# Performance work log

Hardware: AMD Instinct MI355X
Metric: run time of the kernel (lower is better)

The kernel has to match this reference:

```python
import jax, jax.numpy as jnp
import numpy as np
import math

GR = 24
NUM_TDFS = 6
DK = 32
F = 512
BN_UNITS = 192  # max(512*6 // 16, 16)
GROUPS = 4      # mk_norm_2d(24, 'gn') -> largest divisor of 24 in range(ceil(sqrt(24)),2,-1) = 4
EPS = 1e-5


def group_norm(x, w, b):
    # x: [B, C, H, W]; GroupNorm(GROUPS, C)
    B, C, H, W = x.shape
    xg = x.reshape(B, GROUPS, C // GROUPS, H, W)
    mu = xg.mean(axis=(2, 3, 4), keepdims=True)
    var = xg.var(axis=(2, 3, 4), keepdims=True)
    xn = ((xg - mu) * jax.lax.rsqrt(var + EPS)).reshape(B, C, H, W)
    return xn * w[None, :, None, None] + b[None, :, None, None]


def conv_block(x, w, b, gw, gb):
    # Conv2d 3x3 same padding, then GroupNorm, then ReLU
    y = jax.lax.conv_general_dilated(
        x, w, window_strides=(1, 1), padding=((1, 1), (1, 1)),
        dimension_numbers=('NCHW', 'OIHW', 'NCHW')) + b[None, :, None, None]
    return jax.nn.relu(group_norm(y, gw, gb))


def setup_inputs() -> dict:
    key = jax.random.key(0)
    ks = jax.random.split(key, 16)
    B, C_in, T = 4, 24, 128

    def glorot(k, shape, fan_in):
        return jax.random.normal(k, shape, jnp.float32) * (1.0 / math.sqrt(fan_in))

    inp = {
        'x': jax.random.normal(ks[0], (B, C_in, T, F), jnp.float32),
        'c': jax.random.normal(ks[1], (B, 32), jnp.float32),
        # TFC dense conv stack: in-channels 24, 48, 72 -> gr=24 each
        'conv_w0': glorot(ks[2], (GR, 24, 3, 3), 24 * 9), 'conv_b0': jnp.zeros((GR,), jnp.float32),
        'gn_w0': jnp.ones((GR,), jnp.float32), 'gn_b0': jnp.zeros((GR,), jnp.float32),
        'conv_w1': glorot(ks[3], (GR, 48, 3, 3), 48 * 9), 'conv_b1': jnp.zeros((GR,), jnp.float32),
        'gn_w1': jnp.ones((GR,), jnp.float32), 'gn_b1': jnp.zeros((GR,), jnp.float32),
        'conv_w2': glorot(ks[4], (GR, 72, 3, 3), 72 * 9), 'conv_b2': jnp.zeros((GR,), jnp.float32),
        'gn_w2': jnp.ones((GR,), jnp.float32), 'gn_b2': jnp.zeros((GR,), jnp.float32),
        # TDF bottleneck MLP (bias=False): f -> bn_units -> f*num_tdfs
        'tdf_w1': glorot(ks[5], (BN_UNITS, F), F),
        'tdf_gn1_w': jnp.ones((GR,), jnp.float32), 'tdf_gn1_b': jnp.zeros((GR,), jnp.float32),
        'tdf_w2': glorot(ks[6], (F * NUM_TDFS, BN_UNITS), BN_UNITS),
        'tdf_gn2_w': jnp.ones((GR,), jnp.float32), 'tdf_gn2_b': jnp.zeros((GR,), jnp.float32),
        # routing path
        'wq': glorot(ks[7], (DK, 32), 32), 'bq': jnp.zeros((DK,), jnp.float32),
        'keys': jax.random.normal(ks[8], (DK, NUM_TDFS), jnp.float32),
    }
    return inp


def reference(x, c,
              conv_w0, conv_b0, gn_w0, gn_b0,
              conv_w1, conv_b1, gn_w1, gn_b1,
              conv_w2, conv_b2, gn_w2, gn_b2,
              tdf_w1, tdf_gn1_w, tdf_gn1_b,
              tdf_w2, tdf_gn2_w, tdf_gn2_b,
              wq, bq, keys):
    # ---- TFC: densely connected conv blocks ----
    feat = conv_block(x, conv_w0, conv_b0, gn_w0, gn_b0)          # [B,gr,T,F]
    cat = jnp.concatenate([feat, x], axis=1)                      # [B,48,T,F]
    feat = conv_block(cat, conv_w1, conv_b1, gn_w1, gn_b1)
    cat = jnp.concatenate([feat, cat], axis=1)                    # [B,72,T,F]
    x_ = conv_block(cat, conv_w2, conv_b2, gn_w2, gn_b2)          # [B,gr,T,F]

    # ---- TDF bank: f -> bn_units -> f*num_tdfs (bias-free MLP with GN+ReLU) ----
    h = jnp.einsum('bctf,uf->bctu', x_, tdf_w1)                   # [B,gr,T,bn_units]
    h = jax.nn.relu(group_norm(h, tdf_gn1_w, tdf_gn1_b))
    h = jnp.einsum('bctu,ou->bcto', h, tdf_w2)                    # [B,gr,T,f*num_tdfs]
    h = jax.nn.relu(group_norm(h, tdf_gn2_w, tdf_gn2_b))
    B, gr, T, _ = h.shape
    value = h.reshape(B, gr, T, F, NUM_TDFS)                      # [B,gr,T,f,n]

    # ---- LaSAFT attention over TDF 'experts' ----
    q = c @ wq.T + bq                                             # [B,dk]
    att = jax.nn.softmax((q @ keys) / math.sqrt(DK), axis=-1)     # [B,n]
    mixed = jnp.einsum('bctfn,bn->bctf', value, att)              # [B,gr,T,f]
    return x_ + mixed
```

## Files before the change

kernel.cpp:

```cpp
#include <hip/hip_runtime.h>
#include <hip/hip_bf16.h>

typedef unsigned short u16;
typedef unsigned int u32;

#define Tn 128
#define Fn 512
#define HWc (Tn*Fn)
#define EPS 1e-5f

using bf16x8 = __attribute__((ext_vector_type(8))) short;
using f32x4  = __attribute__((ext_vector_type(4))) float;

__device__ __forceinline__ float b2f(u16 x){ return __uint_as_float(((u32)x)<<16); }
__device__ __forceinline__ u16 f2b(float f){
  __hip_bfloat16 h = __float2bfloat16(f);
  return *reinterpret_cast<u16*>(&h);
}

__device__ __forceinline__ void gload16(const u16* g, u16* l){
  __builtin_amdgcn_global_load_lds((const __attribute__((address_space(1))) void*)g,
                                   (__attribute__((address_space(3))) void*)l, 16, 0, 0);
}

__global__ void zero_stats2(float* a, float* b){
  int i = threadIdx.x;
  if (i < 128) a[i] = 0.f;
  else if (i < 160) b[i-128] = 0.f;
}

__global__ __launch_bounds__(256) void border_zero(u16* __restrict__ p, int CS){
  int b = blockIdx.y;
  u16* base = p + (long)b*130*514*CS;
  int rowN = 514*CS;
  for (int i = blockIdx.x*256 + threadIdx.x; i < rowN; i += gridDim.x*256){
    base[i] = 0;
    base[(long)129*rowN + i] = 0;
  }
  int colN = 128*CS;
  for (int i = blockIdx.x*256 + threadIdx.x; i < colN; i += gridDim.x*256){
    int row = 1 + i/CS, ch = i - (i/CS)*CS;
    base[((long)row*514 + 0)*CS + ch] = 0;
    base[((long)row*514 + 513)*CS + ch] = 0;
  }
}

__global__ __launch_bounds__(256) void cvt_f2b(const float* __restrict__ src, u16* __restrict__ dst){
  int i = (blockIdx.x*256 + threadIdx.x)*4;
  float4 v = *(const float4*)(src + i);
  ushort4 o;
  o.x=f2b(v.x); o.y=f2b(v.y); o.z=f2b(v.z); o.w=f2b(v.w);
  *(ushort4*)(dst + i) = o;
}

__global__ __launch_bounds__(256)
void prep_wr(const float* __restrict__ w, u16* __restrict__ wr,
             int CIN, int cs, int cof, int KP){
  int i = blockIdx.x*256 + threadIdx.x;
  int tot = 96*KP;
  if (i >= tot) return;
  int e  = i & 7;
  int r  = (i >> 3) & 15;
  int h  = (i >> 7) & 1;
  int q  = (i >> 8) & 3;
  int rest = i >> 10;
  int NK = KP >> 5;
  int ks = rest % NK, dt = rest / NK;
  int o = h*16 + r;
  int k = ks*32 + q*8 + e;
  float v = 0.f;
  int g = cof + k, df = g/cs, ch = g - df*cs;
  if (o < 24 && df < 3 && ch >= cof && ch < cof+CIN)
    v = w[((o*CIN + (ch-cof))*3 + dt)*3 + df];
  wr[i] = f2b(v);
}

__global__ __launch_bounds__(256)
void copy_x2(const float* __restrict__ x, u16* __restrict__ b72p, u16* __restrict__ xc24){
  __shared__ u16 sh[24][520];
  int t = blockIdx.x & 127, b = blockIdx.x >> 7;
  const float* src = x + ((long)(b*24)*128 + t)*512;
  for (int c=0; c<24; c++){
    float2 v = *(const float2*)(src + (long)c*65536 + threadIdx.x*2);
    sh[c][threadIdx.x*2]   = f2b(v.x);
    sh[c][threadIdx.x*2+1] = f2b(v.y);
  }
  __syncthreads();
  long r72 = ((long)(b*130 + t+1))*514*72;
  long r24 = ((long)(b*130 + t+1))*514*24;
  for (int i = threadIdx.x; i < 1536; i += 256){
    int f = i/3, c0 = (i%3)*8;
    union {int4 q; u16 u[8];} o;
    #pragma unroll
    for (int j=0;j<8;j++) o.u[j] = sh[c0+j][f];
    *(int4*)(b72p + r72 + (long)(f+1)*72 + 48 + c0) = o.q;
    *(int4*)(xc24 + r24 + (long)(f+1)*24 + c0) = o.q;
  }
}

template<int KP, int CS>
__global__ __launch_bounds__(256)
void conv_mfma(const u16* __restrict__ X, int coff, const u16* __restrict__ WR,
               const float* __restrict__ bias, u16* __restrict__ Y,
               float* __restrict__ raw){
  constexpr int NK = KP/32;
  __shared__ u16 WS[3*32*KP];
  __shared__ float ssum[4][32], ssq[4][32];
  __shared__ float g24s[24], g24q[24];
  __shared__ __align__(16) u16 Ysh[128*24];
  int bid = (blockIdx.x & 7)*64 + (blockIdx.x >> 3);
  int b = bid >> 7, t = bid & 127;
  int tid = threadIdx.x, wid = tid >> 6, l = tid & 63;
  int r = l & 15, q = l >> 4;

  for (int i = tid*8; i < 3*32*KP; i += 2048)
    *(int4*)(WS + i) = *(const int4*)(WR + i);

  float bv0 = bias[r];
  float bv1 = (r < 8) ? bias[16+r] : 0.f;
  float s0=0,q0=0,s1=0,q1=0;
  __syncthreads();

  #pragma unroll
  for (int fi=0; fi<4; fi++){
    int f0w = fi*128 + wid*32;
    f32x4 acc[2][2] = {};
    #pragma unroll
    for (int dt=0; dt<3; dt++){
      const u16* Ab = X + ((long)((b*130 + t+dt)*514 + f0w + r))*CS + coff + q*8;
      bf16x8 a[2][NK];
      #pragma unroll
      for (int ks=0; ks<NK; ks++){
        a[0][ks] = *(const bf16x8*)(Ab + ks*32);
        a[1][ks] = *(const bf16x8*)(Ab + (long)16*CS + ks*32);
      }
      #pragma unroll
      for (int ks=0; ks<NK; ks++){
        const u16* Bb = WS + ((dt*NK + ks)*4 + q)*256 + r*8;
        bf16x8 b0 = *(const bf16x8*)(Bb);
        bf16x8 b1 = *(const bf16x8*)(Bb + 128);
        acc[0][0] = __builtin_amdgcn_mfma_f32_16x16x32_bf16(a[0][ks],b0,acc[0][0],0,0,0);
        acc[0][1] = __builtin_amdgcn_mfma_f32_16x16x32_bf16(a[0][ks],b1,acc[0][1],0,0,0);
        acc[1][0] = __builtin_amdgcn_mfma_f32_16x16x32_bf16(a[1][ks],b0,acc[1][0],0,0,0);
        acc[1][1] = __builtin_amdgcn_mfma_f32_16x16x32_bf16(a[1][ks],b1,acc[1][1],0,0,0);
      }
    }
    #pragma unroll
    for (int m=0;m<2;m++){
      #pragma unroll
      for (int j=0;j<4;j++){
        acc[m][0][j] += bv0; acc[m][1][j] += bv1;
        s0 += acc[m][0][j]; q0 += acc[m][0][j]*acc[m][0][j];
        s1 += acc[m][1][j]; q1 += acc[m][1][j]*acc[m][1][j];
      }
    }
    __syncthreads();
    #pragma unroll
    for (int m=0;m<2;m++){
      int fr = wid*32 + m*16 + q*4;
      #pragma unroll
      for (int j=0;j<4;j++){
        Ysh[(fr+j)*24 + r] = f2b(acc[m][0][j]);
        if (r < 8) Ysh[(fr+j)*24 + 16 + r] = f2b(acc[m][1][j]);
      }
    }
    __syncthreads();
    long Yb = ((long)((b*128 + t)*512) + fi*128)*24;
    const int4* sp = (const int4*)Ysh;
    for (int i = tid; i < 384; i += 256)
      *(int4*)(Y + Yb + (long)i*8) = sp[i];
  }

  #pragma unroll
  for (int off=16; off<=32; off<<=1){
    s0 += __shfl_xor(s0, off, 64); q0 += __shfl_xor(q0, off, 64);
    s1 += __shfl_xor(s1, off, 64); q1 += __shfl_xor(q1, off, 64);
  }
  if (q == 0){
    ssum[wid][r] = s0;     ssq[wid][r] = q0;
    ssum[wid][16+r] = s1;  ssq[wid][16+r] = q1;
  }
  __syncthreads();
  if (tid < 24){
    g24s[tid] = ssum[0][tid]+ssum[1][tid]+ssum[2][tid]+ssum[3][tid];
    g24q[tid] = ssq[0][tid]+ssq[1][tid]+ssq[2][tid]+ssq[3][tid];
  }
  __syncthreads();
  if (tid < 4){
    float as=0, aq=0;
    #pragma unroll
    for (int j=0;j<6;j++){ as += g24s[tid*6+j]; aq += g24q[tid*6+j]; }
    atomicAdd(&raw[b*4+tid], as);
    atomicAdd(&raw[16+b*4+tid], aq);
  }
}

__global__ __launch_bounds__(256)
void norm_relu_nhwc(const u16* __restrict__ Y, u16* __restrict__ dst, int coff,
                    const float* __restrict__ raw, const float* __restrict__ gw,
                    const float* __restrict__ gb, float invN){
  __shared__ float sA[24], sB[24];
  int bb = blockIdx.x / 768;
  if (threadIdx.x < 24){
    int g = bb*4 + threadIdx.x/6;
    float m = raw[g]*invN;
    float var = raw[16+g]*invN - m*m;
    float is = rsqrtf(var + EPS);
    float sc = is*gw[threadIdx.x];
    sA[threadIdx.x] = sc;
    sB[threadIdx.x] = gb[threadIdx.x] - m*sc;
  }
  __syncthreads();
  long e = ((long)blockIdx.x*256 + threadIdx.x)*8;
  int c0 = (int)(e % 24);
  long fi = e / 24;
  int f = (int)(fi & 511);
  int bt = (int)(fi >> 9); int t = bt & 127, b = bt >> 7;
  union {int4 q; u16 u[8];} pk; pk.q = *(const int4*)(Y + e);
  union {int4 q; u16 u[8];} o;
  #pragma unroll
  for (int j=0;j<8;j++){
    float v = b2f(pk.u[j])*sA[c0+j] + sB[c0+j];
    o.u[j] = f2b(v>0.f?v:0.f);
  }
  *(int4*)(dst + ((long)(b*130 + t+1)*514 + (f+1))*72 + coff + c0) = o.q;
}

__global__ __launch_bounds__(256)
void norm_relu_chw(const u16* __restrict__ Y, u16* __restrict__ xr,
                   const float* __restrict__ raw, const float* __restrict__ gw,
                   const float* __restrict__ gb, float invN){
  __shared__ u16 sh[24][520];
  __shared__ float sA[24], sB[24];
  int t = blockIdx.x & 127, b = blockIdx.x >> 7;
  if (threadIdx.x < 24){
    int g = b*4 + threadIdx.x/6;
    float m = raw[g]*invN;
    float var = raw[16+g]*invN - m*m;
    float is = rsqrtf(var + EPS);
    float sc = is*gw[threadIdx.x];
    sA[threadIdx.x] = sc;
    sB[threadIdx.x] = gb[threadIdx.x] - m*sc;
  }
  __syncthreads();
  const u16* src = Y + ((long)(b*128+t))*12288;
  for (int i = threadIdx.x; i < 1536; i += 256){
    int e = i*8; int c0 = e % 24; int f = e / 24;
    union {int4 q; u16 u[8];} pk; pk.q = *(const int4*)(src + e);
    #pragma unroll
    for (int j=0;j<8;j++){
      float v = b2f(pk.u[j])*sA[c0+j] + sB[c0+j];
      sh[c0+j][f] = f2b(v>0.f?v:0.f);
    }
  }
  __syncthreads();
  for (int i = threadIdx.x; i < 1536; i += 256){
    int c = i >> 6, fq = (i & 63)*8;
    union {int4 q; u16 u[8];} o;
    #pragma unroll
    for (int j=0;j<8;j++) o.u[j] = sh[c][fq+j];
    *(int4*)(xr + ((long)((b*24+c)*128 + t))*512 + fq) = o.q;
  }
}

__global__ __launch_bounds__(256)
void norm_chw(u16* __restrict__ h, const float* __restrict__ raw,
              const float* __restrict__ gw, const float* __restrict__ gb, float invN){
  __shared__ float s_sc, s_off;
  int bc = blockIdx.x / 12;
  if (threadIdx.x == 0){
    int b = bc/24, c = bc%24;
    int g = b*4 + c/6;
    float m = raw[g]*invN;
    float var = raw[16+g]*invN - m*m;
    float is = rsqrtf(var + EPS);
    float sc = is*gw[c];
    s_sc = sc;
    s_off = gb[c] - m*sc;
  }
  __syncthreads();
  float sc = s_sc, off = s_off;
  long e = ((long)blockIdx.x*256 + threadIdx.x)*8;
  union {int4 q; u16 u[8];} pk; pk.q = *(const int4*)(h + e);
  #pragma unroll
  for (int j=0;j<8;j++){ float v = b2f(pk.u[j])*sc + off; pk.u[j] = f2b(v>0.f?v:0.f); }
  *(int4*)(h + e) = pk.q;
}

template<int NF, bool STORE>
__global__ __launch_bounds__(256)
void gemm_lds(const u16* __restrict__ A, const u16* __restrict__ Bt, u16* __restrict__ C,
              int N, int K, int NBX, float* __restrict__ raw){
  constexpr int BN = NF*32;
  constexpr int BNP = BN + 4;
  constexpr int ABUF = 128*32;
  constexpr int BBUF = BN*32;
  __shared__ __align__(16) u16 SH[3*(ABUF+BBUF)];
  u16* Asb = SH;
  u16* Bsb = SH + 3*ABUF;
  int tid = threadIdx.x, wid = tid >> 6, l = tid & 63;
  int r = l & 15, q = l >> 4;
  int wr = wid >> 1, wc = wid & 1;
  int chunk = gridDim.x >> 3;
  int lin = (blockIdx.x & 7)*chunk + (blockIdx.x >> 3);
  int bx = lin % NBX, by = lin / NBX;
  long m0 = (long)by*128;
  int n0 = bx*BN;

  int arow[2], ach[2], aslot[2];
  #pragma unroll
  for (int j=0;j<2;j++){
    int idx = (wid*2+j)*64 + l;
    aslot[j] = idx*8;
    arow[j]  = ((idx>>6)<<4) | (idx & 15);
    ach[j]   = ((idx>>4) & 3)*8;
  }
  int brow[NF/2], bch[NF/2], bslot[NF/2];
  #pragma unroll
  for (int j=0;j<NF/2;j++){
    int idx = (wid*(NF/2)+j)*64 + l;
    bslot[j] = idx*8;
    brow[j]  = ((idx>>6)<<4) | (idx & 15);
    bch[j]   = ((idx>>4) & 3)*8;
  }

  f32x4 acc[4][NF];
  #pragma unroll
  for (int mf=0;mf<4;mf++)
    #pragma unroll
    for (int nf=0;nf<NF;nf++) acc[mf][nf] = (f32x4){0.f,0.f,0.f,0.f};

  int nt = K >> 5;
  #pragma unroll
  for (int j=0;j<2;j++)    gload16(A  + (m0+arow[j])*K + ach[j], Asb + aslot[j]);
  #pragma unroll
  for (int j=0;j<NF/2;j++) gload16(Bt + (long)(n0+brow[j])*K + bch[j], Bsb + bslot[j]);
  #pragma unroll
  for (int j=0;j<2;j++)    gload16(A  + (m0+arow[j])*K + 32 + ach[j], Asb + ABUF + aslot[j]);
  #pragma unroll
  for (int j=0;j<NF/2;j++) gload16(Bt + (long)(n0+brow[j])*K + 32 + bch[j], Bsb + BBUF + bslot[j]);

  int c0 = 0;
  for (int kt=0; kt<nt; kt++){
    if constexpr (NF==4) asm volatile("s_waitcnt vmcnt(4)" ::: "memory");
    else                 asm volatile("s_waitcnt vmcnt(3)" ::: "memory");
    __builtin_amdgcn_s_barrier();
    __builtin_amdgcn_sched_barrier(0);
    if (kt+2 < nt){
      int c2 = c0+2; if (c2>=3) c2-=3;
      int ko = (kt+2)*32;
      #pragma unroll
      for (int j=0;j<2;j++)    gload16(A  + (m0+arow[j])*K + ko + ach[j], Asb + c2*ABUF + aslot[j]);
      #pragma unroll
      for (int j=0;j<NF/2;j++) gload16(Bt + (long)(n0+brow[j])*K + ko + bch[j], Bsb + c2*BBUF + bslot[j]);
    }
    const u16* Ac = Asb + c0*ABUF;
    const u16* Bc = Bsb + c0*BBUF;
    bf16x8 af[4], bfv[NF];
    #pragma unroll
    for (int mf=0;mf<4;mf++) af[mf]  = *(const bf16x8*)(Ac + (((wr*4+mf)*4 + q)*16 + r)*8);
    #pragma unroll
    for (int nf=0;nf<NF;nf++) bfv[nf] = *(const bf16x8*)(Bc + (((wc*NF+nf)*4 + q)*16 + r)*8);
    #pragma unroll
    for (int mf=0;mf<4;mf++)
      #pragma unroll
      for (int nf=0;nf<NF;nf++)
        acc[mf][nf] = __builtin_amdgcn_mfma_f32_16x16x32_bf16(af[mf], bfv[nf], acc[mf][nf], 0,0,0);
    c0 = (c0+1==3) ? 0 : c0+1;
  }

  float s=0.f, ss=0.f;
  #pragma unroll
  for (int mf=0;mf<4;mf++)
    #pragma unroll
    for (int nf=0;nf<NF;nf++)
      #pragma unroll
      for (int j=0;j<4;j++){ float v = acc[mf][nf][j]; s += v; ss += v*v; }
  #pragma unroll
  for (int off=32; off>0; off>>=1){ s += __shfl_down(s,off,64); ss += __shfl_down(ss,off,64); }
  __shared__ float rs[4], rss[4];
  if (l==0){ rs[wid]=s; rss[wid]=ss; }
  __syncthreads();
  if (tid==0){
    int bc = (int)(m0 >> 7);
    int g = (bc/24)*4 + (bc%24)/6;
    atomicAdd(&raw[g],    rs[0]+rs[1]+rs[2]+rs[3]);
    atomicAdd(&raw[16+g], rss[0]+rss[1]+rss[2]+rss[3]);
  }

  if constexpr (STORE){
    #pragma unroll
    for (int mf=0;mf<4;mf++){
      int row = wr*64 + mf*16 + q*4;
      #pragma unroll
      for (int nf=0;nf<NF;nf++){
        int col = wc*(NF*16) + nf*16 + r;
        #pragma unroll
        for (int j=0;j<4;j++)
          SH[(row+j)*BNP + col] = f2b(acc[mf][nf][j]);
      }
    }
    __syncthreads();
    constexpr int RPT = BN/16;
    #pragma unroll
    for (int k=0;k<RPT;k++){
      int j = tid + k*256;
      int row = j / (BN/8), col8 = (j % (BN/8))*8;
      *(int4*)(C + (m0+row)*N + n0 + col8) = *(const int4*)(SH + row*BNP + col8);
    }
  }
}

__global__ void attention_kernel(const float* __restrict__ c, const float* __restrict__ wq,
                                 const float* __restrict__ bq, const float* __restrict__ keys,
                                 float* __restrict__ att){
  __shared__ float q[4][32];
  __shared__ float s[4][6];
  int t = threadIdx.x;
  if (t < 128){
    int b = t >> 5, k = t & 31;
    float a = bq[k];
    for (int j=0;j<32;j++) a += c[b*32+j] * wq[k*32+j];
    q[b][k] = a;
  }
  __syncthreads();
  if (t < 24){
    int b = t/6, n = t%6;
    float a = 0.f;
    for (int k=0;k<32;k++) a += q[b][k]*keys[k*6+n];
    s[b][n] = a * 0.17677669529663689f;
  }
  __syncthreads();
  if (t < 4){
    float mx = -1e30f;
    for (int n=0;n<6;n++) mx = fmaxf(mx, s[t][n]);
    float e[6], sm=0.f;
    for (int n=0;n<6;n++){ e[n]=expf(s[t][n]-mx); sm+=e[n]; }
    for (int n=0;n<6;n++) att[t*6+n] = e[n]/sm;
  }
}

__global__ __launch_bounds__(256)
void final_mix(const u16* __restrict__ h2, const u16* __restrict__ xr,
               const float* __restrict__ raw, const float* __restrict__ gw,
               const float* __restrict__ gb, float invN,
               const float* __restrict__ att, float* __restrict__ out){
  __shared__ float s_sc, s_off, s_att[6];
  int bc0 = blockIdx.x / 64;
  int c  = bc0 % 24, b = bc0 / 24;
  if (threadIdx.x == 0){
    int g = b*4 + c/6;
    float m = raw[g]*invN;
    float var = raw[16+g]*invN - m*m;
    float is = rsqrtf(var + EPS);
    float sc = is*gw[c];
    s_sc = sc;
    s_off = gb[c] - m*sc;
  }
  if (threadIdx.x < 6) s_att[threadIdx.x] = att[b*6+threadIdx.x];
  __syncthreads();
  float sc = s_sc, off = s_off;
  float a[6];
  #pragma unroll
  for (int n=0;n<6;n++) a[n] = s_att[n];

  int gid = blockIdx.x*256 + threadIdx.x;
  int fq = gid & 127;
  int t  = (gid >> 7) & 127;
  int bc = gid >> 14;

  long hbase = (((long)bc*Tn + t))*3072 + (long)fq*24;
  union { int4 v[3]; u16 u[24]; } hv;
  const int4* hp = (const int4*)(h2 + hbase);
  hv.v[0]=hp[0]; hv.v[1]=hp[1]; hv.v[2]=hp[2];

  long xbase = (((long)bc*Tn + t))*Fn + (long)fq*4;
  union { unsigned long long q; u16 u[4]; } xv;
  xv.q = *(const unsigned long long*)(xr + xbase);

  float4 ov;
  float* op = &ov.x;
  #pragma unroll
  for (int j=0;j<4;j++){
    float accv = b2f(xv.u[j]);
    #pragma unroll
    for (int n=0;n<6;n++){
      float hvf = b2f(hv.u[j*6+n])*sc + off;
      hvf = hvf > 0.f ? hvf : 0.f;
      accv += hvf * a[n];
    }
    op[j] = accv;
  }
  *(float4*)(out + xbase) = ov;
}

extern "C" void kernel_launch(void* const* d_in, const int* in_sizes, int n_in,
                              void* d_out, int out_size, void* d_ws, size_t ws_size,
                              hipStream_t stream){
  const float* x   = (const float*)d_in[0];
  const float* c   = (const float*)d_in[1];
  const float* cw0 = (const float*)d_in[2];  const float* cb0 = (const float*)d_in[3];
  const float* gw0 = (const float*)d_in[4];  const float* gb0 = (const float*)d_in[5];
  const float* cw1 = (const float*)d_in[6];  const float* cb1 = (const float*)d_in[7];
  const float* gw1 = (const float*)d_in[8];  const float* gb1 = (const float*)d_in[9];
  const float* cw2 = (const float*)d_in[10]; const float* cb2 = (const float*)d_in[11];
  const float* gw2 = (const float*)d_in[12]; const float* gb2 = (const float*)d_in[13];
  const float* tw1 = (const float*)d_in[14]; const float* tg1w= (const float*)d_in[15]; const float* tg1b=(const float*)d_in[16];
  const float* tw2 = (const float*)d_in[17]; const float* tg2w= (const float*)d_in[18]; const float* tg2b=(const float*)d_in[19];
  const float* wqp = (const float*)d_in[20]; const float* bqp = (const float*)d_in[21]; const float* keys=(const float*)d_in[22];

  char* ws = (char*)d_ws;
  u16*   xr     = (u16*)(ws + 0);
  u16*   h1     = (u16*)(ws + 12582912);
  u16*   tw1b   = (u16*)(ws + 17301504);
  u16*   tw2b   = (u16*)(ws + 17498112);
  float* stats5 = (float*)(ws + 18677760);
  float* att    = (float*)(ws + 18678656);
  u16*   h2     = (u16*)(ws + 18680832);
  u16*   Y      = (u16*)(ws + 18680832);
  u16*   b72p   = (u16*)(ws + 31263744);
  u16*   xc24   = (u16*)(ws + 69752064);
  float* stats14= (float*)(ws + 82581760);
  u16*   wr0    = (u16*)(ws + 82585344);
  u16*   wr1    = (u16*)(ws + 82603776);
  u16*   wr2    = (u16*)(ws + 82640640);

  border_zero<<<dim3(32,4),256,0,stream>>>(b72p, 72);
  border_zero<<<dim3(16,4),256,0,stream>>>(xc24, 24);
  zero_stats2<<<1,256,0,stream>>>(stats14, stats5);

  prep_wr<<<36,256,0,stream>>>(cw0, wr0, 24, 24, 0, 96);
  prep_wr<<<72,256,0,stream>>>(cw1, wr1, 48, 72, 24, 192);
  prep_wr<<<84,256,0,stream>>>(cw2, wr2, 72, 72, 0, 224);
  cvt_f2b<<<96,256,0,stream>>>(tw1, tw1b);
  cvt_f2b<<<576,256,0,stream>>>(tw2, tw2b);
  copy_x2<<<512,256,0,stream>>>(x, b72p, xc24);
  attention_kernel<<<1,128,0,stream>>>(c, wqp, bqp, keys, att);

  conv_mfma<96,24><<<512,256,0,stream>>>(xc24, 0, wr0, cb0, Y, stats14+0);
  norm_relu_nhwc<<<3072,256,0,stream>>>(Y, b72p, 24, stats14+0, gw0, gb0, 1.f/393216.f);

  conv_mfma<192,72><<<512,256,0,stream>>>(b72p, 24, wr1, cb1, Y, stats14+32);
  norm_relu_nhwc<<<3072,256,0,stream>>>(Y, b72p, 0, stats14+32, gw1, gb1, 1.f/393216.f);

  conv_mfma<224,72><<<512,256,0,stream>>>(b72p, 0, wr2, cb2, Y, stats14+64);
  norm_relu_chw<<<512,256,0,stream>>>(Y, xr, stats14+64, gw2, gb2, 1.f/393216.f);

  gemm_lds<2,true><<<288,256,0,stream>>>(xr, tw1b, h1, 192, 512, 3, stats14+96);
  norm_chw<<<1152,256,0,stream>>>(h1, stats14+96, tg1w, tg1b, 1.f/147456.f);

  gemm_lds<4,true><<<2304,256,0,stream>>>(h1, tw2b, h2, 3072, 192, 24, stats5);

  final_mix<<<6144,256,0,stream>>>(h2, xr, stats5, tg2w, tg2b, 1.f/2359296.f, att, (float*)d_out);
}
```

Before: 230.7 us.

## Add specialized second TDF GEMM keeping A tile resident and streaming B ring buffer

Replaces the generic LDS GEMM for the second TDF projection with a dedicated kernel. Each block holds its 64x192 A tile in LDS, streams B through a four-slot ring buffer with manual vmcnt waits, and walks six 64-column N chunks. Output is written straight from registers instead of staged through LDS, and group-norm statistics are accumulated on the fly. The intent is to reuse A across N chunks, cut reloads and overlap loads with MFMA work. The unstaged global stores are less coalesced, and the hand-tuned wait counts are fragile.

```diff
diff --git a/kernel.cpp b/kernel.cpp
--- a/kernel.cpp
+++ b/kernel.cpp
@@ -411,6 +411,94 @@
   }
 }
 
+__global__ __launch_bounds__(256)
+void gemm2_ns(const u16* __restrict__ A, const u16* __restrict__ Bt, u16* __restrict__ C,
+              float* __restrict__ raw){
+  __shared__ __align__(16) u16 As[24*512];
+  __shared__ __align__(16) u16 Bring[4*2048];
+  __shared__ float rs[4], rss[4];
+  const int K = 192, N = 3072;
+  int tid = threadIdx.x, wid = tid >> 6, l = tid & 63;
+  int r = l & 15, q = l >> 4;
+  int wr = wid >> 1, wc = wid & 1;
+  int lin = (blockIdx.x & 7)*192 + (blockIdx.x >> 3);
+  int by = lin >> 3, bx2 = lin & 7;
+  long m0 = (long)by*64;
+  int nbase = bx2*384;
+
+  #pragma unroll
+  for (int j=0;j<6;j++){
+    int e = j*4 + wid;
+    int hi = e/6, ks = e%6;
+    gload16(A + (m0 + hi*16 + r)*K + ks*32 + q*8, As + e*512 + l*8);
+  }
+  #pragma unroll
+  for (int p=0;p<3;p++)
+    gload16(Bt + (long)(nbase + wid*16 + r)*K + p*32 + q*8, Bring + p*2048 + tid*8);
+
+  float s=0.f, ss=0.f;
+  f32x4 acc[2][2];
+  #pragma unroll
+  for (int mf=0;mf<2;mf++)
+    #pragma unroll
+    for (int nf=0;nf<2;nf++) acc[mf][nf] = (f32x4){0.f,0.f,0.f,0.f};
+
+  for (int t=0; t<36; t++){
+    int ks = t % 6;
+    if (t >= 6 && ks < 3) asm volatile("s_waitcnt vmcnt(18)" ::: "memory");
+    else                  asm volatile("s_waitcnt vmcnt(2)"  ::: "memory");
+    __builtin_amdgcn_s_barrier();
+    __builtin_amdgcn_sched_barrier(0);
+    if (t+3 < 36){
+      int t3 = t+3;
+      int jn3 = t3/6, ks3 = t3%6;
+      gload16(Bt + (long)(nbase + jn3*64 + wid*16 + r)*K + ks3*32 + q*8,
+              Bring + (t3&3)*2048 + tid*8);
+    }
+    const u16* Bs = Bring + (t&3)*2048;
+    bf16x8 af[2], bfv[2];
+    #pragma unroll
+    for (int mf=0;mf<2;mf++) af[mf]  = *(const bf16x8*)(As + ((wr*2+mf)*6 + ks)*512 + (q*16+r)*8);
+    #pragma unroll
+    for (int nf=0;nf<2;nf++) bfv[nf] = *(const bf16x8*)(Bs + ((wc*2+nf)*64 + q*16 + r)*8);
+    #pragma unroll
+    for (int mf=0;mf<2;mf++)
+      #pragma unroll
+      for (int nf=0;nf<2;nf++)
+        acc[mf][nf] = __builtin_amdgcn_mfma_f32_16x16x32_bf16(af[mf], bfv[nf], acc[mf][nf], 0,0,0);
+    if (ks == 5){
+      int jn = t/6;
+      long ncol = nbase + jn*64;
+      #pragma unroll
+      for (int mf=0;mf<2;mf++){
+        long rowb = m0 + wr*32 + mf*16 + q*4;
+        #pragma unroll
+        for (int nf=0;nf<2;nf++){
+          long col = ncol + wc*32 + nf*16 + r;
+          #pragma unroll
+          for (int j=0;j<4;j++){
+            float v = acc[mf][nf][j];
+            s += v; ss += v*v;
+            C[(rowb+j)*N + col] = f2b(v);
+          }
+          acc[mf][nf] = (f32x4){0.f,0.f,0.f,0.f};
+        }
+      }
+    }
+  }
+
+  #pragma unroll
+  for (int off=32; off>0; off>>=1){ s += __shfl_down(s,off,64); ss += __shfl_down(ss,off,64); }
+  if (l==0){ rs[wid]=s; rss[wid]=ss; }
+  __syncthreads();
+  if (tid==0){
+    int bc = (int)(m0 >> 7);
+    int g = (bc/24)*4 + (bc%24)/6;
+    atomicAdd(&raw[g],    rs[0]+rs[1]+rs[2]+rs[3]);
+    atomicAdd(&raw[16+g], rss[0]+rss[1]+rss[2]+rss[3]);
+  }
+}
+
 __global__ void attention_kernel(const float* __restrict__ c, const float* __restrict__ wq,
                                  const float* __restrict__ bq, const float* __restrict__ keys,
                                  float* __restrict__ att){
@@ -549,7 +637,7 @@
   gemm_lds<2,true><<<288,256,0,stream>>>(xr, tw1b, h1, 192, 512, 3, stats14+96);
   norm_chw<<<1152,256,0,stream>>>(h1, stats14+96, tg1w, tg1b, 1.f/147456.f);
 
-  gemm_lds<4,true><<<2304,256,0,stream>>>(h1, tw2b, h2, 3072, 192, 24, stats5);
+  gemm2_ns<<<1536,256,0,stream>>>(h1, tw2b, h2, stats5);
 
   final_mix<<<6144,256,0,stream>>>(h2, xr, stats5, tg2w, tg2b, 1.f/2359296.f, att, (float*)d_out);
 }
```

After: 245.7 us. +6.5%, slower.
